# Optimization experiments

Measured on AMD Instinct MI355X. Metric: run time of the kernel, lower is better.

Reference implementation:

```python
import jax, jax.numpy as jnp
import numpy as np

N = 100000
IN_C, HID_C, OUT_C = 128, 128, 64
E = 1600000


def setup_inputs() -> dict:
    key = jax.random.key(0)
    ks = jax.random.split(key, 8)
    x = jax.random.normal(ks[0], (N, IN_C), dtype=jnp.float32)
    edge_index = jax.random.randint(ks[1], (2, E), 0, N, dtype=jnp.int64)
    def glorot(k, fan_in, fan_out):
        lim = np.sqrt(6.0 / (fan_in + fan_out)).astype(np.float32)
        return jax.random.uniform(k, (fan_in, fan_out), jnp.float32, -lim, lim)
    return {
        "x": x,
        "edge_index": edge_index,
        "W1l": glorot(ks[2], IN_C, HID_C),   # lin_l: aggregated neighbors
        "W1r": glorot(ks[3], IN_C, HID_C),   # lin_r: root/self
        "b1": jnp.zeros((HID_C,), jnp.float32),
        "W2l": glorot(ks[4], HID_C, OUT_C),
        "W2r": glorot(ks[5], HID_C, OUT_C),
        "b2": jnp.zeros((OUT_C,), jnp.float32),
    }


def _sage_conv(x, src, dst, Wl, Wr, b):
    # mean aggregation over incoming edges: gather source feats, segment-sum at dst
    msg_sum = jax.ops.segment_sum(x[src], dst, num_segments=N)          # [N, C_in]
    deg = jax.ops.segment_sum(jnp.ones((src.shape[0],), x.dtype), dst,
                              num_segments=N)                           # [N]
    mean = msg_sum / jnp.clip(deg, 1.0, None)[:, None]
    return mean @ Wl + x @ Wr + b


def reference(x, edge_index, W1l, W1r, b1, W2l, W2r, b2):
    src, dst = edge_index[0], edge_index[1]
    h = jax.nn.relu(_sage_conv(x, src, dst, W1l, W1r, b1))
    out = _sage_conv(h, src, dst, W2l, W2r, b2)
    return out
```

## Files before the change

### kernel.cpp

```cpp
#include <hip/hip_runtime.h>
#include <type_traits>


constexpr int K = 128;
constexpr int EB = 4096;
constexpr int CAP = 8192;

typedef __bf16 bf16x2 __attribute__((ext_vector_type(2)));
typedef __bf16 bf16x4 __attribute__((ext_vector_type(4)));
typedef __bf16 bf16x8 __attribute__((ext_vector_type(8)));
typedef float f32x4 __attribute__((ext_vector_type(4)));
typedef float f32x2 __attribute__((ext_vector_type(2)));


__device__ __forceinline__ unsigned char to_fp8(float v) {
#if __has_builtin(__builtin_amdgcn_cvt_pk_fp8_f32)
  int p = __builtin_amdgcn_cvt_pk_fp8_f32(v, v, 0, false);
  return (unsigned char)(p & 0xff);
#else
  unsigned u = __builtin_bit_cast(unsigned, v);
  unsigned s = (u >> 24) & 0x80u;
  float a = fabsf(v);
  if (a > 448.f) a = 448.f;
  unsigned bits;
  if (a < 0.015625f) {
    bits = (unsigned)(a * 512.f + 0.5f);
  } else {
    unsigned b = __builtin_bit_cast(unsigned, a);
    b += ((b >> 20) & 1) + 0x0007FFFF;
    unsigned e = (b >> 23) - 120;
    bits = (e << 3) | ((b >> 20) & 7);
    if (bits > 0x7E) bits = 0x7E;
  }
  return (unsigned char)(s | bits);
#endif
}

__device__ __forceinline__ f32x2 from_fp8x2(unsigned short u) {
#if __has_builtin(__builtin_amdgcn_cvt_pk_f32_fp8)
  return __builtin_amdgcn_cvt_pk_f32_fp8((int)u, false);
#else
  f32x2 r;
  unsigned b0 = u & 0xff, b1 = (u >> 8) & 0xff;
  unsigned e0 = (b0 >> 3) & 15, m0 = b0 & 7;
  unsigned e1 = (b1 >> 3) & 15, m1 = b1 & 7;
  float v0 = e0 ? __builtin_bit_cast(float, ((e0 + 120) << 23) | (m0 << 20))
              : (float)m0 * 0.001953125f;
  float v1 = e1 ? __builtin_bit_cast(float, ((e1 + 120) << 23) | (m1 << 20))
              : (float)m1 * 0.001953125f;
  r[0] = (b0 & 0x80) ? -v0 : v0;
  r[1] = (b1 & 0x80) ? -v1 : v1;
  return r;
#endif
}

__device__ __forceinline__ f32x2 fp8x2_lo(unsigned v) {
#if __has_builtin(__builtin_amdgcn_cvt_pk_f32_fp8)
  return __builtin_amdgcn_cvt_pk_f32_fp8((int)v, false);
#else
  return from_fp8x2((unsigned short)(v & 0xffffu));
#endif
}

__device__ __forceinline__ f32x2 fp8x2_hi(unsigned v) {
#if __has_builtin(__builtin_amdgcn_cvt_pk_f32_fp8)
  return __builtin_amdgcn_cvt_pk_f32_fp8((int)v, true);
#else
  return from_fp8x2((unsigned short)(v >> 16));
#endif
}


template <int COLS>
__global__ __launch_bounds__(512, 4) void k_scatter_gemm(
    const int* __restrict__ src, const int* __restrict__ dst,
    int* __restrict__ bucketCount, unsigned* __restrict__ recs,
    int E, int n, int nB, int nscat,
    int* __restrict__ tileCtr, const float* __restrict__ X,
    const float* __restrict__ Wa, const float* __restrict__ Wb,
    unsigned char* __restrict__ outA, __bf16* __restrict__ outB, int ntiles) {
  constexpr int LD = 136;
  constexpr int NI = COLS / 64;
  __shared__ __bf16 As[2][64 * LD];
  __shared__ int shT;

  int bid = blockIdx.x;
  int tid = threadIdx.x;

  if (bid < nscat) {
    int* cur = (int*)As;
    for (int i = tid; i < nB; i += 512) cur[i] = 0;
    __syncthreads();
    int base = bid * EB, endE = min(base + EB, E);
    for (int e = base + tid; e < endE; e += 512) {
      int d = dst[e];
      if ((unsigned)d < (unsigned)n) atomicAdd(&cur[d >> 8], 1);
    }
    __syncthreads();
    for (int i = tid; i < nB; i += 512) {
      int c = cur[i];
      cur[i] = c ? atomicAdd(&bucketCount[i], c) : 0;
    }
    __syncthreads();
    for (int e = base + tid; e < endE; e += 512) {
      int d = dst[e];
      if ((unsigned)d < (unsigned)n) {
        int s = min(max(src[e], 0), n - 1);
        int b = d >> 8;
        int pos = min(atomicAdd(&cur[b], 1), CAP - 1);
        recs[(long)b * CAP + pos] = ((unsigned)s << 8) | (unsigned)(d & 255);
      }
    }
    __syncthreads();
  }

  int w = tid >> 6, lane = tid & 63;
  int m = lane & 15, quad = lane >> 4;
  int panel = w >> 2;
  int wcol = (w & 3) * (16 * NI);
  const float* Wsrc = panel ? Wb : Wa;

  bf16x8 bq[4][NI];
#pragma unroll
  for (int kc = 0; kc < 4; ++kc)
#pragma unroll
    for (int ni = 0; ni < NI; ++ni)
#pragma unroll
      for (int e = 0; e < 8; ++e)
        bq[kc][ni][e] = (__bf16)Wsrc[(kc * 32 + quad * 8 + e) * COLS + (wcol + ni * 16 + m)];

  float4 ra[4];
  auto load_tile = [&](int t) {
    long row0 = (long)t * 64;
#pragma unroll
    for (int it = 0; it < 4; ++it) {
      int i = tid + it * 512;
      int r = i >> 5, c4 = (i & 31) << 2;
      long row = row0 + r;
      float4 v = make_float4(0.f, 0.f, 0.f, 0.f);
      if (row < n) v = *(const float4*)(X + row * K + c4);
      ra[it] = v;
    }
  };
  auto write_tile = [&](int buf) {
#pragma unroll
    for (int it = 0; it < 4; ++it) {
      int i = tid + it * 512;
      int r = i >> 5, c4 = (i & 31) << 2;
      bf16x4 bb;
      bb[0] = (__bf16)ra[it].x; bb[1] = (__bf16)ra[it].y;
      bb[2] = (__bf16)ra[it].z; bb[3] = (__bf16)ra[it].w;
      *(bf16x4*)&As[buf][r * LD + c4] = bb;
    }
  };

  if (tid == 0) shT = atomicAdd(tileCtr, 1);
  __syncthreads();
  int t = shT;
  if (t < ntiles) load_tile(t);

#pragma unroll
  for (int kc = 0; kc < 4; ++kc)
#pragma unroll
    for (int ni = 0; ni < NI; ++ni)
      asm volatile("" :: "v"(bq[kc][ni]));

  int buf = 0;
  while (t < ntiles) {
    write_tile(buf);
    __syncthreads();
    if (tid == 0) shT = atomicAdd(tileCtr, 1);
    __syncthreads();
    int tn = shT;
    if (tn < ntiles) load_tile(tn);

    f32x4 acc[4][NI];
#pragma unroll
    for (int mi = 0; mi < 4; ++mi)
#pragma unroll
      for (int ni = 0; ni < NI; ++ni) acc[mi][ni] = (f32x4){0.f, 0.f, 0.f, 0.f};

#pragma unroll
    for (int kc = 0; kc < 4; ++kc) {
      int ko = kc * 32 + quad * 8;
      bf16x8 af[4];
#pragma unroll
      for (int mi = 0; mi < 4; ++mi)
        af[mi] = *(const bf16x8*)&As[buf][(mi * 16 + m) * LD + ko];
#pragma unroll
      for (int mi = 0; mi < 4; ++mi)
#pragma unroll
        for (int ni = 0; ni < NI; ++ni)
          acc[mi][ni] = __builtin_amdgcn_mfma_f32_16x16x32_bf16(af[mi], bq[kc][ni], acc[mi][ni], 0, 0, 0);
    }

    long row0 = (long)t * 64;
#pragma unroll
    for (int mi = 0; mi < 4; ++mi) {
#pragma unroll
      for (int r = 0; r < 4; ++r) {
        long grow = row0 + mi * 16 + quad * 4 + r;
        if (grow < n) {
#pragma unroll
          for (int ni = 0; ni < NI; ++ni) {
            long idx = grow * COLS + wcol + ni * 16 + m;
            float v = acc[mi][ni][r];
            if (panel == 0) outA[idx] = to_fp8(v);
            else            outB[idx] = (__bf16)v;
          }
        }
      }
    }
    t = tn;
    buf ^= 1;
  }
}

__global__ __launch_bounds__(256) void k_bfill(const unsigned* __restrict__ recs,
                                               const int* __restrict__ bucketCount,
                                               int* __restrict__ rowptr,
                                               int* __restrict__ col, int n) {
  __shared__ int degl[256];
  __shared__ int incl[256];
  __shared__ int red[256];
  int b = blockIdx.x, t = threadIdx.x;

  int partial = 0;
  for (int i = t; i < b; i += 256) partial += bucketCount[i];
  red[t] = partial;
  __syncthreads();
  for (int off = 128; off > 0; off >>= 1) {
    if (t < off) red[t] += red[t + off];
    __syncthreads();
  }
  int rbeg = red[0];
  int cnt = bucketCount[b];
  const unsigned* rbase = recs + (long)b * CAP;
  __syncthreads();

  degl[t] = 0;
  __syncthreads();
  for (int i = t; i < cnt; i += 256)
    atomicAdd(&degl[rbase[i] & 255], 1);
  __syncthreads();
  incl[t] = degl[t];
  __syncthreads();
  for (int off = 1; off < 256; off <<= 1) {
    int v = (t >= off) ? incl[t - off] : 0;
    __syncthreads();
    incl[t] += v;
    __syncthreads();
  }
  int excl = incl[t] - degl[t];
  int node = b * 256 + t;
  if (node <= n) rowptr[node] = rbeg + excl;
  __syncthreads();
  degl[t] = rbeg + excl;
  __syncthreads();
  for (int i = t; i < cnt; i += 256) {
    unsigned r = rbase[i];
    int pos = atomicAdd(&degl[r & 255], 1);
    col[pos] = (int)(r >> 8);
  }
}


template <int COLS, typename TIN>
__global__ __launch_bounds__(512, 4) void k_gemm_fused(const TIN* __restrict__ X,
                                                       const float* __restrict__ Wa,
                                                       const float* __restrict__ Wb,
                                                       unsigned char* __restrict__ outA,
                                                       __bf16* __restrict__ outB,
                                                       int nrows, int ntiles) {
  constexpr int LD = 136;
  constexpr int NI = COLS / 64;
  constexpr bool FP32IN = std::is_same_v<TIN, float>;
  __shared__ __bf16 As[2][64 * LD];

  int tid = threadIdx.x;
  int w = tid >> 6, lane = tid & 63;
  int m = lane & 15, quad = lane >> 4;
  int panel = w >> 2;
  int wcol = (w & 3) * (16 * NI);
  const float* Wsrc = panel ? Wb : Wa;

  bf16x8 bq[4][NI];
#pragma unroll
  for (int kc = 0; kc < 4; ++kc)
#pragma unroll
    for (int ni = 0; ni < NI; ++ni)
#pragma unroll
      for (int e = 0; e < 8; ++e)
        bq[kc][ni][e] = (__bf16)Wsrc[(kc * 32 + quad * 8 + e) * COLS + (wcol + ni * 16 + m)];

  float4 ra[4];
  bf16x8 rb[2];

  auto load_tile = [&](int t) {
    long row0 = (long)t * 64;
    if constexpr (FP32IN) {
#pragma unroll
      for (int it = 0; it < 4; ++it) {
        int i = tid + it * 512;
        int r = i >> 5, c4 = (i & 31) << 2;
        long row = row0 + r;
        float4 v = make_float4(0.f, 0.f, 0.f, 0.f);
        if (row < nrows) v = *(const float4*)(X + row * K + c4);
        ra[it] = v;
      }
    } else {
#pragma unroll
      for (int it = 0; it < 2; ++it) {
        int i = tid + it * 512;
        int r = i >> 4, c8 = (i & 15) << 3;
        long row = row0 + r;
        bf16x8 v = {};
        if (row < nrows) v = *(const bf16x8*)(X + row * K + c8);
        rb[it] = v;
      }
    }
  };

  auto write_tile = [&](int buf) {
    if constexpr (FP32IN) {
#pragma unroll
      for (int it = 0; it < 4; ++it) {
        int i = tid + it * 512;
        int r = i >> 5, c4 = (i & 31) << 2;
        bf16x4 bb;
        bb[0] = (__bf16)ra[it].x; bb[1] = (__bf16)ra[it].y;
        bb[2] = (__bf16)ra[it].z; bb[3] = (__bf16)ra[it].w;
        *(bf16x4*)&As[buf][r * LD + c4] = bb;
      }
    } else {
#pragma unroll
      for (int it = 0; it < 2; ++it) {
        int i = tid + it * 512;
        int r = i >> 4, c8 = (i & 15) << 3;
        *(bf16x8*)&As[buf][r * LD + c8] = rb[it];
      }
    }
  };

  int t = (int)blockIdx.x;
  int stride = (int)gridDim.x;
  if (t < ntiles) load_tile(t);

#pragma unroll
  for (int kc = 0; kc < 4; ++kc)
#pragma unroll
    for (int ni = 0; ni < NI; ++ni)
      asm volatile("" :: "v"(bq[kc][ni]));

  int buf = 0;
  while (t < ntiles) {
    write_tile(buf);
    __syncthreads();
    int tn = t + stride;
    if (tn < ntiles) load_tile(tn);

    f32x4 acc[4][NI];
#pragma unroll
    for (int mi = 0; mi < 4; ++mi)
#pragma unroll
      for (int ni = 0; ni < NI; ++ni) acc[mi][ni] = (f32x4){0.f, 0.f, 0.f, 0.f};

#pragma unroll
    for (int kc = 0; kc < 4; ++kc) {
      int ko = kc * 32 + quad * 8;
      bf16x8 af[4];
#pragma unroll
      for (int mi = 0; mi < 4; ++mi)
        af[mi] = *(const bf16x8*)&As[buf][(mi * 16 + m) * LD + ko];
#pragma unroll
      for (int mi = 0; mi < 4; ++mi)
#pragma unroll
        for (int ni = 0; ni < NI; ++ni)
          acc[mi][ni] = __builtin_amdgcn_mfma_f32_16x16x32_bf16(af[mi], bq[kc][ni], acc[mi][ni], 0, 0, 0);
    }

    long row0 = (long)t * 64;
#pragma unroll
    for (int mi = 0; mi < 4; ++mi) {
#pragma unroll
      for (int r = 0; r < 4; ++r) {
        long grow = row0 + mi * 16 + quad * 4 + r;
        if (grow < nrows) {
#pragma unroll
          for (int ni = 0; ni < NI; ++ni) {
            long idx = grow * COLS + wcol + ni * 16 + m;
            float v = acc[mi][ni][r];
            if (panel == 0) outA[idx] = to_fp8(v);
            else            outB[idx] = (__bf16)v;
          }
        }
      }
    }
    t = tn;
    buf ^= 1;
  }
}


template <bool RELU>
__global__ __launch_bounds__(256) void k_agg128(const unsigned char* __restrict__ Y,
                                                const __bf16* __restrict__ XR,
                                                const float* __restrict__ bias,
                                                const int* __restrict__ rowptr,
                                                const int* __restrict__ col,
                                                __bf16* __restrict__ out, int nnodes) {
  int wave = threadIdx.x >> 6, lane = threadIdx.x & 63;
  int quarter = lane >> 4, l = lane & 15;
  int sb = lane & 48;
  int n = blockIdx.x * 16 + wave * 4 + quarter;
  bool valid = n < nnodes;
  int beg = 0, end = 0;
  if (valid) {
    beg = rowptr[n];
    end = rowptr[n + 1];
  }
  int co = l * 8;
  const unsigned char* Yc = Y + co;

  f32x2 av0 = {0.f, 0.f}, av1 = {0.f, 0.f}, av2 = {0.f, 0.f}, av3 = {0.f, 0.f};

  for (int base = beg; base < end; base += 16) {
    int cnt = min(end - base, 16);
    int idx = (l < cnt) ? col[base + l] : 0;
    int j = 0;
    for (; j + 3 < cnt; j += 4) {
      long s0 = (unsigned)__shfl(idx, sb + j);
      long s1 = (unsigned)__shfl(idx, sb + j + 1);
      long s2 = (unsigned)__shfl(idx, sb + j + 2);
      long s3 = (unsigned)__shfl(idx, sb + j + 3);
      uint2 v0 = *(const uint2*)(Yc + s0 * 128);
      uint2 v1 = *(const uint2*)(Yc + s1 * 128);
      uint2 v2 = *(const uint2*)(Yc + s2 * 128);
      uint2 v3 = *(const uint2*)(Yc + s3 * 128);
      av0 += fp8x2_lo(v0.x); av1 += fp8x2_hi(v0.x);
      av2 += fp8x2_lo(v0.y); av3 += fp8x2_hi(v0.y);
      av0 += fp8x2_lo(v1.x); av1 += fp8x2_hi(v1.x);
      av2 += fp8x2_lo(v1.y); av3 += fp8x2_hi(v1.y);
      av0 += fp8x2_lo(v2.x); av1 += fp8x2_hi(v2.x);
      av2 += fp8x2_lo(v2.y); av3 += fp8x2_hi(v2.y);
      av0 += fp8x2_lo(v3.x); av1 += fp8x2_hi(v3.x);
      av2 += fp8x2_lo(v3.y); av3 += fp8x2_hi(v3.y);
    }
    for (; j < cnt; ++j) {
      long s = (unsigned)__shfl(idx, sb + j);
      uint2 v = *(const uint2*)(Yc + s * 128);
      av0 += fp8x2_lo(v.x); av1 += fp8x2_hi(v.x);
      av2 += fp8x2_lo(v.y); av3 += fp8x2_hi(v.y);
    }
  }

  if (valid) {
    float inv = 1.f / (float)max(end - beg, 1);
    bf16x8 xv = *(const bf16x8*)(XR + (long)n * 128 + co);
    f32x4 b0 = *(const f32x4*)(bias + co);
    f32x4 b1 = *(const f32x4*)(bias + co + 4);
    float r0 = av0[0] * inv + (float)xv[0] + b0[0];
    float r1 = av0[1] * inv + (float)xv[1] + b0[1];
    float r2 = av1[0] * inv + (float)xv[2] + b0[2];
    float r3 = av1[1] * inv + (float)xv[3] + b0[3];
    float r4 = av2[0] * inv + (float)xv[4] + b1[0];
    float r5 = av2[1] * inv + (float)xv[5] + b1[1];
    float r6 = av3[0] * inv + (float)xv[6] + b1[2];
    float r7 = av3[1] * inv + (float)xv[7] + b1[3];
    if (RELU) {
      r0 = fmaxf(r0, 0.f); r1 = fmaxf(r1, 0.f);
      r2 = fmaxf(r2, 0.f); r3 = fmaxf(r3, 0.f);
      r4 = fmaxf(r4, 0.f); r5 = fmaxf(r5, 0.f);
      r6 = fmaxf(r6, 0.f); r7 = fmaxf(r7, 0.f);
    }
    bf16x8 o;
    o[0] = (__bf16)r0; o[1] = (__bf16)r1; o[2] = (__bf16)r2; o[3] = (__bf16)r3;
    o[4] = (__bf16)r4; o[5] = (__bf16)r5; o[6] = (__bf16)r6; o[7] = (__bf16)r7;
    *(bf16x8*)(out + (long)n * 128 + co) = o;
  }
}

__global__ __launch_bounds__(256) void k_agg64(const unsigned char* __restrict__ Y,
                                               const __bf16* __restrict__ XR,
                                               const float* __restrict__ bias,
                                               const int* __restrict__ rowptr,
                                               const int* __restrict__ col,
                                               float* __restrict__ out, int nnodes) {
  int wave = threadIdx.x >> 6, lane = threadIdx.x & 63;
  int quarter = lane >> 4, l = lane & 15;
  int sb = lane & 48;
  int n = blockIdx.x * 16 + wave * 4 + quarter;
  bool valid = n < nnodes;
  int beg = 0, end = 0;
  if (valid) {
    beg = rowptr[n];
    end = rowptr[n + 1];
  }
  int co = l * 4;
  const unsigned char* Yc = Y + co;

  f32x2 av0 = {0.f, 0.f}, av1 = {0.f, 0.f};

  for (int base = beg; base < end; base += 16) {
    int cnt = min(end - base, 16);
    int idx = (l < cnt) ? col[base + l] : 0;
    int j = 0;
    for (; j + 3 < cnt; j += 4) {
      long s0 = (unsigned)__shfl(idx, sb + j);
      long s1 = (unsigned)__shfl(idx, sb + j + 1);
      long s2 = (unsigned)__shfl(idx, sb + j + 2);
      long s3 = (unsigned)__shfl(idx, sb + j + 3);
      unsigned v0 = *(const unsigned*)(Yc + s0 * 64);
      unsigned v1 = *(const unsigned*)(Yc + s1 * 64);
      unsigned v2 = *(const unsigned*)(Yc + s2 * 64);
      unsigned v3 = *(const unsigned*)(Yc + s3 * 64);
      av0 += fp8x2_lo(v0); av1 += fp8x2_hi(v0);
      av0 += fp8x2_lo(v1); av1 += fp8x2_hi(v1);
      av0 += fp8x2_lo(v2); av1 += fp8x2_hi(v2);
      av0 += fp8x2_lo(v3); av1 += fp8x2_hi(v3);
    }
    for (; j < cnt; ++j) {
      long s = (unsigned)__shfl(idx, sb + j);
      unsigned v = *(const unsigned*)(Yc + s * 64);
      av0 += fp8x2_lo(v); av1 += fp8x2_hi(v);
    }
  }

  if (valid) {
    float inv = 1.f / (float)max(end - beg, 1);
    bf16x4 xv = *(const bf16x4*)(XR + (long)n * 64 + co);
    f32x4 bv = *(const f32x4*)(bias + co);
    f32x4 r;
    r[0] = av0[0] * inv + (float)xv[0] + bv[0];
    r[1] = av0[1] * inv + (float)xv[1] + bv[1];
    r[2] = av1[0] * inv + (float)xv[2] + bv[2];
    r[3] = av1[1] * inv + (float)xv[3] + bv[3];
    *(f32x4*)(out + (long)n * 64 + co) = r;
  }
}


extern "C" void kernel_launch(void* const* d_in, const int* in_sizes, int n_in,
                              void* d_out, int out_size, void* d_ws, size_t ws_size,
                              hipStream_t stream) {
  const float* x   = (const float*)d_in[0];
  const int*   ei  = (const int*)d_in[1];
  const float* W1l = (const float*)d_in[2];
  const float* W1r = (const float*)d_in[3];
  const float* b1  = (const float*)d_in[4];
  const float* W2l = (const float*)d_in[5];
  const float* W2r = (const float*)d_in[6];
  const float* b2  = (const float*)d_in[7];
  float* out = (float*)d_out;

  int N = in_sizes[0] / K;
  int E = in_sizes[1] / 2;
  const int* src = ei;
  const int* dst = ei + E;

  int nB = (N + 255) >> 8;
  int nblk = (E + EB - 1) / EB;

  char* ws = (char*)d_ws;
  size_t off = 0;
  auto alloc = [&](size_t bytes) {
    void* p = ws + off;
    off = (off + bytes + 255) & ~(size_t)255;
    return p;
  };
  int*      rowptr      = (int*)alloc(((size_t)N + 2) * 4);
  int*      col         = (int*)alloc((size_t)E * 4);
  int*      meta        = (int*)alloc(((size_t)nB + 80) * 4);
  unsigned* recs        = (unsigned*)alloc((size_t)nB * CAP * 4);
  unsigned char* y1     = (unsigned char*)alloc((size_t)N * 128);
  __bf16*   xr          = (__bf16*)alloc((size_t)N * 128 * 2);
  __bf16*   h           = (__bf16*)alloc((size_t)N * 128 * 2);
  unsigned char* y2 = y1;
  __bf16*   hr = xr;

  int* bucketCount = meta;
  int* tileCtr     = meta + nB + 16;

  int ntiles = (N + 63) / 64;
  int gpers = ntiles < 512 ? ntiles : 512;

  hipMemsetAsync(meta, 0, ((size_t)nB + 80) * 4, stream);
  k_scatter_gemm<128><<<nblk + gpers, 512, 0, stream>>>(
      src, dst, bucketCount, recs, E, N, nB, nblk,
      tileCtr, x, W1l, W1r, y1, xr, ntiles);

  k_bfill<<<nB, 256, 0, stream>>>(recs, bucketCount, rowptr, col, N);
  k_agg128<true><<<(N + 15) / 16, 256, 0, stream>>>(y1, xr, b1, rowptr, col, h, N);

  k_gemm_fused<64, __bf16><<<gpers, 512, 0, stream>>>(h, W2l, W2r, y2, hr, N, ntiles);

  k_agg64<<<(N + 15) / 16, 256, 0, stream>>>(y2, hr, b2, rowptr, col, out, N);
}
```

Before: 241.9 us.

## Fuse bucket-fill CSR build into scatter+GEMM kernel via global completion counter

Moves the per-bucket CSR construction (rowptr/col fill) from a separate k_bfill launch into the tail of the fused scatter+GEMM kernel. Blocks spin on a global scatterDone counter until all scatter blocks finish, then dynamically grab buckets through a fillCtr atomic and build rowptr/col with 512 threads. This removes one kernel launch and its boundary drain. In exchange it adds a grid-wide spin-wait, which relies on all scatter blocks being resident or already finished to avoid deadlock.

```diff
diff --git a/kernel.cpp b/kernel.cpp
--- a/kernel.cpp
+++ b/kernel.cpp
@@ -72,13 +72,16 @@
 
 
 template <int COLS>
-__global__ __launch_bounds__(512, 4) void k_scatter_gemm(
+__global__ __launch_bounds__(512, 4) void k_fused1(
     const int* __restrict__ src, const int* __restrict__ dst,
     int* __restrict__ bucketCount, unsigned* __restrict__ recs,
     int E, int n, int nB, int nscat,
-    int* __restrict__ tileCtr, const float* __restrict__ X,
-    const float* __restrict__ Wa, const float* __restrict__ Wb,
-    unsigned char* __restrict__ outA, __bf16* __restrict__ outB, int ntiles) {
+    int* __restrict__ tileCtr, int* __restrict__ fillCtr,
+    int* __restrict__ scatterDone,
+    const float* __restrict__ X, const float* __restrict__ Wa,
+    const float* __restrict__ Wb, unsigned char* __restrict__ outA,
+    __bf16* __restrict__ outB, int ntiles,
+    int* __restrict__ rowptr, int* __restrict__ col) {
   constexpr int LD = 136;
   constexpr int NI = COLS / 64;
   __shared__ __bf16 As[2][64 * LD];
@@ -112,155 +115,171 @@
       }
     }
     __syncthreads();
-  }
-
-  int w = tid >> 6, lane = tid & 63;
-  int m = lane & 15, quad = lane >> 4;
-  int panel = w >> 2;
-  int wcol = (w & 3) * (16 * NI);
-  const float* Wsrc = panel ? Wb : Wa;
-
-  bf16x8 bq[4][NI];
-#pragma unroll
-  for (int kc = 0; kc < 4; ++kc)
-#pragma unroll
-    for (int ni = 0; ni < NI; ++ni)
-#pragma unroll
-      for (int e = 0; e < 8; ++e)
-        bq[kc][ni][e] = (__bf16)Wsrc[(kc * 32 + quad * 8 + e) * COLS + (wcol + ni * 16 + m)];
-
-  float4 ra[4];
-  auto load_tile = [&](int t) {
-    long row0 = (long)t * 64;
-#pragma unroll
-    for (int it = 0; it < 4; ++it) {
-      int i = tid + it * 512;
-      int r = i >> 5, c4 = (i & 31) << 2;
-      long row = row0 + r;
-      float4 v = make_float4(0.f, 0.f, 0.f, 0.f);
-      if (row < n) v = *(const float4*)(X + row * K + c4);
-      ra[it] = v;
-    }
-  };
-  auto write_tile = [&](int buf) {
-#pragma unroll
-    for (int it = 0; it < 4; ++it) {
-      int i = tid + it * 512;
-      int r = i >> 5, c4 = (i & 31) << 2;
-      bf16x4 bb;
-      bb[0] = (__bf16)ra[it].x; bb[1] = (__bf16)ra[it].y;
-      bb[2] = (__bf16)ra[it].z; bb[3] = (__bf16)ra[it].w;
-      *(bf16x4*)&As[buf][r * LD + c4] = bb;
-    }
-  };
-
-  if (tid == 0) shT = atomicAdd(tileCtr, 1);
-  __syncthreads();
-  int t = shT;
-  if (t < ntiles) load_tile(t);
-
-#pragma unroll
-  for (int kc = 0; kc < 4; ++kc)
-#pragma unroll
-    for (int ni = 0; ni < NI; ++ni)
-      asm volatile("" :: "v"(bq[kc][ni]));
-
-  int buf = 0;
-  while (t < ntiles) {
-    write_tile(buf);
-    __syncthreads();
+    __threadfence();
+    if (tid == 0) atomicAdd(scatterDone, 1);
+    __syncthreads();
+  }
+
+  {
+    int w = tid >> 6, lane = tid & 63;
+    int m = lane & 15, quad = lane >> 4;
+    int panel = w >> 2;
+    int wcol = (w & 3) * (16 * NI);
+    const float* Wsrc = panel ? Wb : Wa;
+
+    bf16x8 bq[4][NI];
+#pragma unroll
+    for (int kc = 0; kc < 4; ++kc)
+#pragma unroll
+      for (int ni = 0; ni < NI; ++ni)
+#pragma unroll
+        for (int e = 0; e < 8; ++e)
+          bq[kc][ni][e] = (__bf16)Wsrc[(kc * 32 + quad * 8 + e) * COLS + (wcol + ni * 16 + m)];
+
+    float4 ra[4];
+    auto load_tile = [&](int t) {
+      long row0 = (long)t * 64;
+#pragma unroll
+      for (int it = 0; it < 4; ++it) {
+        int i = tid + it * 512;
+        int r = i >> 5, c4 = (i & 31) << 2;
+        long row = row0 + r;
+        float4 v = make_float4(0.f, 0.f, 0.f, 0.f);
+        if (row < n) v = *(const float4*)(X + row * K + c4);
+        ra[it] = v;
+      }
+    };
+    auto write_tile = [&](int buf) {
+#pragma unroll
+      for (int it = 0; it < 4; ++it) {
+        int i = tid + it * 512;
+        int r = i >> 5, c4 = (i & 31) << 2;
+        bf16x4 bb;
+        bb[0] = (__bf16)ra[it].x; bb[1] = (__bf16)ra[it].y;
+        bb[2] = (__bf16)ra[it].z; bb[3] = (__bf16)ra[it].w;
+        *(bf16x4*)&As[buf][r * LD + c4] = bb;
+      }
+    };
+
     if (tid == 0) shT = atomicAdd(tileCtr, 1);
     __syncthreads();
-    int tn = shT;
-    if (tn < ntiles) load_tile(tn);
-
-    f32x4 acc[4][NI];
-#pragma unroll
-    for (int mi = 0; mi < 4; ++mi)
-#pragma unroll
-      for (int ni = 0; ni < NI; ++ni) acc[mi][ni] = (f32x4){0.f, 0.f, 0.f, 0.f};
-
-#pragma unroll
-    for (int kc = 0; kc < 4; ++kc) {
-      int ko = kc * 32 + quad * 8;
-      bf16x8 af[4];
+    int t = shT;
+    if (t < ntiles) load_tile(t);
+
+#pragma unroll
+    for (int kc = 0; kc < 4; ++kc)
+#pragma unroll
+      for (int ni = 0; ni < NI; ++ni)
+        asm volatile("" :: "v"(bq[kc][ni]));
+
+    int buf = 0;
+    while (t < ntiles) {
+      write_tile(buf);
+      __syncthreads();
+      if (tid == 0) shT = atomicAdd(tileCtr, 1);
+      __syncthreads();
+      int tn = shT;
+      if (tn < ntiles) load_tile(tn);
+
+      f32x4 acc[4][NI];
 #pragma unroll
       for (int mi = 0; mi < 4; ++mi)
-        af[mi] = *(const bf16x8*)&As[buf][(mi * 16 + m) * LD + ko];
-#pragma unroll
-      for (int mi = 0; mi < 4; ++mi)
-#pragma unroll
-        for (int ni = 0; ni < NI; ++ni)
-          acc[mi][ni] = __builtin_amdgcn_mfma_f32_16x16x32_bf16(af[mi], bq[kc][ni], acc[mi][ni], 0, 0, 0);
-    }
-
-    long row0 = (long)t * 64;
-#pragma unroll
-    for (int mi = 0; mi < 4; ++mi) {
-#pragma unroll
-      for (int r = 0; r < 4; ++r) {
-        long grow = row0 + mi * 16 + quad * 4 + r;
-        if (grow < n) {
-#pragma unroll
-          for (int ni = 0; ni < NI; ++ni) {
-            long idx = grow * COLS + wcol + ni * 16 + m;
-            float v = acc[mi][ni][r];
-            if (panel == 0) outA[idx] = to_fp8(v);
-            else            outB[idx] = (__bf16)v;
+#pragma unroll
+        for (int ni = 0; ni < NI; ++ni) acc[mi][ni] = (f32x4){0.f, 0.f, 0.f, 0.f};
+
+#pragma unroll
+      for (int kc = 0; kc < 4; ++kc) {
+        int ko = kc * 32 + quad * 8;
+        bf16x8 af[4];
+#pragma unroll
+        for (int mi = 0; mi < 4; ++mi)
+          af[mi] = *(const bf16x8*)&As[buf][(mi * 16 + m) * LD + ko];
+#pragma unroll
+        for (int mi = 0; mi < 4; ++mi)
+#pragma unroll
+          for (int ni = 0; ni < NI; ++ni)
+            acc[mi][ni] = __builtin_amdgcn_mfma_f32_16x16x32_bf16(af[mi], bq[kc][ni], acc[mi][ni], 0, 0, 0);
+      }
+
+      long row0 = (long)t * 64;
+#pragma unroll
+      for (int mi = 0; mi < 4; ++mi) {
+#pragma unroll
+        for (int r = 0; r < 4; ++r) {
+          long grow = row0 + mi * 16 + quad * 4 + r;
+          if (grow < n) {
+#pragma unroll
+            for (int ni = 0; ni < NI; ++ni) {
+              long idx = grow * COLS + wcol + ni * 16 + m;
+              float v = acc[mi][ni][r];
+              if (panel == 0) outA[idx] = to_fp8(v);
+              else            outB[idx] = (__bf16)v;
+            }
           }
         }
       }
-    }
-    t = tn;
-    buf ^= 1;
-  }
-}
-
-__global__ __launch_bounds__(256) void k_bfill(const unsigned* __restrict__ recs,
-                                               const int* __restrict__ bucketCount,
-                                               int* __restrict__ rowptr,
-                                               int* __restrict__ col, int n) {
-  __shared__ int degl[256];
-  __shared__ int incl[256];
-  __shared__ int red[256];
-  int b = blockIdx.x, t = threadIdx.x;
-
-  int partial = 0;
-  for (int i = t; i < b; i += 256) partial += bucketCount[i];
-  red[t] = partial;
+      t = tn;
+      buf ^= 1;
+    }
+  }
+
+  if (tid == 0) {
+    while (atomicAdd(scatterDone, 0) < nscat) {}
+  }
   __syncthreads();
-  for (int off = 128; off > 0; off >>= 1) {
-    if (t < off) red[t] += red[t + off];
-    __syncthreads();
-  }
-  int rbeg = red[0];
-  int cnt = bucketCount[b];
-  const unsigned* rbase = recs + (long)b * CAP;
-  __syncthreads();
-
-  degl[t] = 0;
-  __syncthreads();
-  for (int i = t; i < cnt; i += 256)
-    atomicAdd(&degl[rbase[i] & 255], 1);
-  __syncthreads();
-  incl[t] = degl[t];
-  __syncthreads();
-  for (int off = 1; off < 256; off <<= 1) {
-    int v = (t >= off) ? incl[t - off] : 0;
-    __syncthreads();
-    incl[t] += v;
-    __syncthreads();
-  }
-  int excl = incl[t] - degl[t];
-  int node = b * 256 + t;
-  if (node <= n) rowptr[node] = rbeg + excl;
-  __syncthreads();
-  degl[t] = rbeg + excl;
-  __syncthreads();
-  for (int i = t; i < cnt; i += 256) {
-    unsigned r = rbase[i];
-    int pos = atomicAdd(&degl[r & 255], 1);
-    col[pos] = (int)(r >> 8);
+  __threadfence();
+
+  int* ish = (int*)As;
+  int* degl = ish;
+  int* incl = ish + 256;
+  int* red  = ish + 512;
+
+  while (true) {
+    __syncthreads();
+    if (tid == 0) shT = atomicAdd(fillCtr, 1);
+    __syncthreads();
+    int b = shT;
+    if (b >= nB) break;
+
+    int partial = 0;
+    for (int i = tid; i < b; i += 512) partial += bucketCount[i];
+    red[tid] = partial;
+    __syncthreads();
+    for (int off = 256; off > 0; off >>= 1) {
+      if (tid < off) red[tid] += red[tid + off];
+      __syncthreads();
+    }
+    int rbeg = red[0];
+    int cnt = bucketCount[b];
+    const unsigned* rbase = recs + (long)b * CAP;
+    __syncthreads();
+
+    if (tid < 256) degl[tid] = 0;
+    __syncthreads();
+    for (int i = tid; i < cnt; i += 512)
+      atomicAdd(&degl[rbase[i] & 255], 1);
+    __syncthreads();
+    if (tid < 256) incl[tid] = degl[tid];
+    __syncthreads();
+    for (int off = 1; off < 256; off <<= 1) {
+      int v = 0;
+      if (tid < 256 && tid >= off) v = incl[tid - off];
+      __syncthreads();
+      if (tid < 256) incl[tid] += v;
+      __syncthreads();
+    }
+    if (tid < 256) {
+      int excl = incl[tid] - degl[tid];
+      int node = b * 256 + tid;
+      if (node <= n) rowptr[node] = rbeg + excl;
+      degl[tid] = rbeg + excl;
+    }
+    __syncthreads();
+    for (int i = tid; i < cnt; i += 512) {
+      unsigned r = rbase[i];
+      int pos = atomicAdd(&degl[r & 255], 1);
+      col[pos] = (int)(r >> 8);
+    }
   }
 }
 
@@ -580,16 +599,18 @@
 
   int* bucketCount = meta;
   int* tileCtr     = meta + nB + 16;
+  int* fillCtr     = meta + nB + 32;
+  int* scatterDone = meta + nB + 48;
 
   int ntiles = (N + 63) / 64;
   int gpers = ntiles < 512 ? ntiles : 512;
 
   hipMemsetAsync(meta, 0, ((size_t)nB + 80) * 4, stream);
-  k_scatter_gemm<128><<<nblk + gpers, 512, 0, stream>>>(
+  k_fused1<128><<<nblk + gpers, 512, 0, stream>>>(
       src, dst, bucketCount, recs, E, N, nB, nblk,
-      tileCtr, x, W1l, W1r, y1, xr, ntiles);
-
-  k_bfill<<<nB, 256, 0, stream>>>(recs, bucketCount, rowptr, col, N);
+      tileCtr, fillCtr, scatterDone,
+      x, W1l, W1r, y1, xr, ntiles, rowptr, col);
+
   k_agg128<true><<<(N + 15) / 16, 256, 0, stream>>>(y1, xr, b1, rowptr, col, h, N);
 
   k_gemm_fused<64, __bf16><<<gpers, 512, 0, stream>>>(h, W2l, W2r, y2, hr, N, ntiles);
```

Result: slower. 598.2 us (+147.3%).
